# Performance work log

Hardware: AMD Instinct MI355X
Metric: run time of the kernel (lower is better)

The kernel has to match this reference:

```python
import jax, jax.numpy as jnp
import numpy as np

B, T, C = 8, 1024, 1024
H, D = 16, 64  # num_heads, head_size

def setup_inputs() -> dict:
    key = jax.random.key(0)
    ks = jax.random.split(key, 6)
    s = C ** -0.5
    return {
        "x": jax.random.normal(ks[0], (B, T, C), dtype=jnp.float32),
        "Wq": jax.random.normal(ks[1], (H, C, D), dtype=jnp.float32) * s,
        "Wk": jax.random.normal(ks[2], (H, C, D), dtype=jnp.float32) * s,
        "Wv": jax.random.normal(ks[3], (H, C, D), dtype=jnp.float32) * s,
        "Wproj": jax.random.normal(ks[4], (H * D, C), dtype=jnp.float32) * ((H * D) ** -0.5),
        "bproj": jnp.zeros((C,), dtype=jnp.float32),
    }

def reference(x, Wq, Wk, Wv, Wproj, bproj):
    # per-head QKV projections, batched over heads via einsum (same math as looped heads)
    q = jnp.einsum('btc,hcd->bhtd', x, Wq)
    k = jnp.einsum('btc,hcd->bhtd', x, Wk)
    v = jnp.einsum('btc,hcd->bhtd', x, Wv)
    scale = D ** -0.5  # k.shape[-1]**-0.5 in original head
    scores = jnp.einsum('bhtd,bhsd->bhts', q, k) * scale  # [B,H,T,T]
    Tn = x.shape[1]
    causal = jnp.tril(jnp.ones((Tn, Tn), dtype=bool))
    scores = jnp.where(causal, scores, jnp.float32(-jnp.inf))
    att = jax.nn.softmax(scores, axis=-1)
    out = jnp.einsum('bhts,bhsd->bhtd', att, v)          # [B,H,T,D]
    out = out.transpose(0, 2, 1, 3).reshape(x.shape[0], Tn, H * D)  # concat heads
    return out @ Wproj + bproj  # dropout is identity at p=0.0
```

## Files before the change

### kernel.cpp

```cpp
#include <hip/hip_runtime.h>
#include <hip/hip_bf16.h>

#define B_ 8
#define T_ 1024
#define C_ 1024
#define H_ 16
#define D_ 64
#define QKVLD 3072

typedef short v8s __attribute__((ext_vector_type(8)));
typedef float v4f __attribute__((ext_vector_type(4)));

__device__ __forceinline__ unsigned short f2b(float f) {
    unsigned int u = __builtin_bit_cast(unsigned int, f);
    unsigned int lsb = (u >> 16) & 1u;
    u += 0x7fffu + lsb;
    return (unsigned short)(u >> 16);
}

__device__ __forceinline__ float fexp2(float x) {
#if __has_builtin(__builtin_amdgcn_exp2f)
    return __builtin_amdgcn_exp2f(x);
#else
    return __expf(x * 0.69314718056f);
#endif
}

#define GLOAD16(gp, lp)                                                          \
    __builtin_amdgcn_global_load_lds(                                            \
        (const __attribute__((address_space(1))) unsigned int*)(gp),             \
        (__attribute__((address_space(3))) unsigned int*)(lp), 16, 0, 0)

#define VMWAIT() __asm__ volatile("s_waitcnt vmcnt(0)" ::: "memory")

__global__ void cast_x_kernel(const float* __restrict__ x, unsigned short* __restrict__ y, int n) {
    int i = (blockIdx.x * 256 + threadIdx.x) * 4;
    if (i < n) {
        float4 v = *(const float4*)(x + i);
        ushort4 o;
        o.x = f2b(v.x); o.y = f2b(v.y); o.z = f2b(v.z); o.w = f2b(v.w);
        *(ushort4*)(y + i) = o;
    }
}

__global__ void transpose_wqkv(const float* __restrict__ Wq, const float* __restrict__ Wk,
                               const float* __restrict__ Wv, unsigned short* __restrict__ WqkvT) {
    int z = blockIdx.y;
    int h = z / 3, part = z % 3;
    const float* src = (part == 0 ? Wq : (part == 1 ? Wk : Wv)) + (size_t)h * C_ * D_;
    int c0 = blockIdx.x * 64;
    __shared__ unsigned short t[64][65];
    for (int i = threadIdx.x; i < 4096; i += 256) {
        int r = i >> 6, d = i & 63;
        t[d][r] = f2b(src[(size_t)(c0 + r) * D_ + d]);
    }
    __syncthreads();
    unsigned short* dst = WqkvT + (size_t)(h * 192 + part * 64) * C_;
    for (int i = threadIdx.x; i < 4096; i += 256) {
        int d = i >> 6, r = i & 63;
        dst[(size_t)d * C_ + c0 + r] = t[d][r];
    }
}

__global__ void transpose_wproj(const float* __restrict__ W, unsigned short* __restrict__ Wt) {
    int k0 = blockIdx.y * 64, n0 = blockIdx.x * 64;
    __shared__ unsigned short t[64][65];
    for (int i = threadIdx.x; i < 4096; i += 256) {
        int r = i >> 6, c = i & 63;
        t[c][r] = f2b(W[(size_t)(k0 + r) * C_ + n0 + c]);
    }
    __syncthreads();
    for (int i = threadIdx.x; i < 4096; i += 256) {
        int n = i >> 6, k = i & 63;
        Wt[(size_t)(n0 + n) * 1024 + k0 + k] = t[n][k];
    }
}

template<int WRITE_MODE>
__global__ __launch_bounds__(256) void gemm_bt(const unsigned short* __restrict__ A,
                                               const unsigned short* __restrict__ Bt,
                                               void* __restrict__ Cout,
                                               const float* __restrict__ bias,
                                               int M, int N, int K) {
    __shared__ unsigned short lA[128 * 32];
    __shared__ unsigned short lB[128 * 32];
    int tid = threadIdx.x;
    int m0 = blockIdx.y * 128, n0 = blockIdx.x * 128;
    int lane = tid & 63, w = tid >> 6;
    int quad = lane >> 4, l16 = lane & 15;
    int wm = w >> 1, wn = w & 1;

    const unsigned short* gA[2];
    const unsigned short* gB[2];
    int ldsOff[2];
    #pragma unroll
    for (int j = 0; j < 2; j++) {
        int c = j * 256 + tid;
        int row = c >> 2;
        int col8 = ((c & 3) ^ ((row >> 1) & 3)) * 8;
        gA[j] = A + (size_t)(m0 + row) * K + col8;
        gB[j] = Bt + (size_t)(n0 + row) * K + col8;
        ldsOff[j] = (j * 256 + w * 64) * 16;
    }
    int rcol = (quad ^ ((l16 >> 1) & 3)) * 8;

    v4f acc[4][4];
    #pragma unroll
    for (int i = 0; i < 4; i++)
        #pragma unroll
        for (int j = 0; j < 4; j++) acc[i][j] = (v4f){0.f, 0.f, 0.f, 0.f};

    for (int k0 = 0; k0 < K; k0 += 32) {
        #pragma unroll
        for (int j = 0; j < 2; j++) {
            GLOAD16(gA[j] + k0, (char*)lA + ldsOff[j]);
            GLOAD16(gB[j] + k0, (char*)lB + ldsOff[j]);
        }
        VMWAIT();
        __syncthreads();
        v8s af[4], bf[4];
        #pragma unroll
        for (int mt = 0; mt < 4; mt++) af[mt] = *(const v8s*)&lA[(wm * 64 + mt * 16 + l16) * 32 + rcol];
        #pragma unroll
        for (int nt = 0; nt < 4; nt++) bf[nt] = *(const v8s*)&lB[(wn * 64 + nt * 16 + l16) * 32 + rcol];
        #pragma unroll
        for (int mt = 0; mt < 4; mt++)
            #pragma unroll
            for (int nt = 0; nt < 4; nt++)
                acc[mt][nt] = __builtin_amdgcn_mfma_f32_16x16x32_bf16(af[mt], bf[nt], acc[mt][nt], 0, 0, 0);
        __syncthreads();
    }
    #pragma unroll
    for (int mt = 0; mt < 4; mt++) {
        #pragma unroll
        for (int nt = 0; nt < 4; nt++) {
            #pragma unroll
            for (int r = 0; r < 4; r++) {
                int row = m0 + wm * 64 + mt * 16 + quad * 4 + r;
                int col = n0 + wn * 64 + nt * 16 + l16;
                float v = acc[mt][nt][r];
                if (WRITE_MODE == 1)
                    ((float*)Cout)[(size_t)row * N + col] = v + bias[col];
                else
                    ((unsigned short*)Cout)[(size_t)row * N + col] = f2b(v);
            }
        }
    }
}

__global__ void transpose_v(const unsigned short* __restrict__ QKV, unsigned short* __restrict__ Vt) {
    int t0 = blockIdx.x * 64;
    int bh = blockIdx.y;
    int b = bh >> 4, h = bh & 15;
    __shared__ unsigned short t[64][65];
    for (int i = threadIdx.x; i < 4096; i += 256) {
        int r = i >> 6, d = i & 63;
        t[d][r] = QKV[(size_t)(b * T_ + t0 + r) * QKVLD + h * 192 + 128 + d];
    }
    __syncthreads();
    for (int i = threadIdx.x; i < 4096; i += 256) {
        int d = i >> 6, r = i & 63;
        Vt[((size_t)bh * 64 + d) * T_ + t0 + r] = t[d][r];
    }
}

__global__ __launch_bounds__(256) void attn_kernel(const unsigned short* __restrict__ QKV,
                                                   const unsigned short* __restrict__ Vt,
                                                   unsigned short* __restrict__ Ob) {
    int bh = blockIdx.x;
    int qt = 7 - blockIdx.y;
    int b = bh >> 4, h = bh & 15;
    int tid = threadIdx.x, lane = tid & 63, w = tid >> 6;
    int quad = lane >> 4, l16 = lane & 15;
    int qg0 = qt * 128 + w * 32;

    __shared__ unsigned short lK[2][2][64][32];
    __shared__ unsigned short lV[2][64][32];
    __shared__ unsigned short lP[4][32][76];

    v8s aq[2][2];
    #pragma unroll
    for (int st = 0; st < 2; st++) {
        const unsigned short* qp = QKV + (size_t)(b * T_ + qg0 + st * 16 + l16) * QKVLD + h * 192;
        aq[st][0] = *(const v8s*)(qp + quad * 8);
        aq[st][1] = *(const v8s*)(qp + 32 + quad * 8);
    }

    const unsigned short* gK[2];
    const unsigned short* gV[2];
    int ldsOff[2];
    #pragma unroll
    for (int j = 0; j < 2; j++) {
        int c = j * 256 + tid;
        int halfp = c >> 8, row = (c >> 2) & 63;
        int col8 = ((c & 3) ^ ((row >> 1) & 3)) * 8;
        gK[j] = QKV + (size_t)(b * T_ + row) * QKVLD + h * 192 + 64 + halfp * 32 + col8;
        gV[j] = Vt + ((size_t)bh * 64 + row) * T_ + halfp * 32 + col8;
        ldsOff[j] = (j * 256 + w * 64) * 16;
    }
    int rcol = (quad ^ ((l16 >> 1) & 3)) * 8;

    v4f accO[2][4];
    float lsum[2][4];
    #pragma unroll
    for (int st = 0; st < 2; st++)
        #pragma unroll
        for (int i = 0; i < 4; i++) { accO[st][i] = (v4f){0.f, 0.f, 0.f, 0.f}; lsum[st][i] = 0.f; }

    int ntiles = 2 * qt + 2;
    const float SC = 0.1803368801f;

    #pragma unroll
    for (int j = 0; j < 2; j++)
        GLOAD16(gK[j], (char*)&lK[0][0][0][0] + ldsOff[j]);

    for (int it = 0; it < ntiles; it++) {
        int cur = it & 1, nxt = cur ^ 1;
        int s0 = it * 64;
        __asm__ volatile("s_waitcnt vmcnt(0)" ::: "memory");
        __asm__ volatile("s_barrier" ::: "memory");
        #pragma unroll
        for (int j = 0; j < 2; j++)
            GLOAD16(gV[j] + s0, (char*)&lV[0][0][0] + ldsOff[j]);
        __asm__ volatile("" ::: "memory");
        {
            int itn = (it + 1 < ntiles) ? it + 1 : it;
            size_t koff = (size_t)itn * 64 * QKVLD;
            #pragma unroll
            for (int j = 0; j < 2; j++)
                GLOAD16(gK[j] + koff, (char*)&lK[nxt][0][0][0] + ldsOff[j]);
        }
        bool act0 = (qg0 + 15 >= s0);
        bool act1 = (qg0 + 31 >= s0);
        if (act1) {
            v4f sf[2][4];
            #pragma unroll
            for (int nt = 0; nt < 4; nt++) {
                v8s bk0 = *(const v8s*)&lK[cur][0][nt * 16 + l16][rcol];
                v8s bk1 = *(const v8s*)&lK[cur][1][nt * 16 + l16][rcol];
                if (act0) {
                    v4f a = (v4f){0.f, 0.f, 0.f, 0.f};
                    a = __builtin_amdgcn_mfma_f32_16x16x32_bf16(aq[0][0], bk0, a, 0, 0, 0);
                    a = __builtin_amdgcn_mfma_f32_16x16x32_bf16(aq[0][1], bk1, a, 0, 0, 0);
                    sf[0][nt] = a;
                }
                v4f a1 = (v4f){0.f, 0.f, 0.f, 0.f};
                a1 = __builtin_amdgcn_mfma_f32_16x16x32_bf16(aq[1][0], bk0, a1, 0, 0, 0);
                a1 = __builtin_amdgcn_mfma_f32_16x16x32_bf16(aq[1][1], bk1, a1, 0, 0, 0);
                sf[1][nt] = a1;
            }
            bool diag = (it >= ntiles - 2);
            #pragma unroll
            for (int st = 0; st < 2; st++) {
                if (st == 0 && !act0) continue;
                if (diag) {
                    #pragma unroll
                    for (int nt = 0; nt < 4; nt++)
                        #pragma unroll
                        for (int r = 0; r < 4; r++) {
                            int sg = s0 + nt * 16 + l16;
                            int qg = qg0 + st * 16 + quad * 4 + r;
                            float p = (sg > qg) ? 0.f : fexp2(sf[st][nt][r] * SC);
                            lsum[st][r] += p;
                            lP[w][st * 16 + quad * 4 + r][nt * 16 + l16] = f2b(p);
                        }
                } else {
                    #pragma unroll
                    for (int nt = 0; nt < 4; nt++)
                        #pragma unroll
                        for (int r = 0; r < 4; r++) {
                            float p = fexp2(sf[st][nt][r] * SC);
                            lsum[st][r] += p;
                            lP[w][st * 16 + quad * 4 + r][nt * 16 + l16] = f2b(p);
                        }
                }
            }
        }
        __asm__ volatile("s_waitcnt vmcnt(2)" ::: "memory");
        __asm__ volatile("s_barrier" ::: "memory");
        __asm__ volatile("s_waitcnt lgkmcnt(0)" ::: "memory");
        if (act1) {
            #pragma unroll
            for (int sc = 0; sc < 2; sc++) {
                v8s ap0, ap1;
                if (act0) ap0 = *(const v8s*)&lP[w][l16][sc * 32 + quad * 8];
                ap1 = *(const v8s*)&lP[w][16 + l16][sc * 32 + quad * 8];
                #pragma unroll
                for (int dt = 0; dt < 4; dt++) {
                    v8s bv = *(const v8s*)&lV[sc][dt * 16 + l16][rcol];
                    if (act0) accO[0][dt] = __builtin_amdgcn_mfma_f32_16x16x32_bf16(ap0, bv, accO[0][dt], 0, 0, 0);
                    accO[1][dt] = __builtin_amdgcn_mfma_f32_16x16x32_bf16(ap1, bv, accO[1][dt], 0, 0, 0);
                }
            }
        }
    }
    #pragma unroll
    for (int st = 0; st < 2; st++)
        #pragma unroll
        for (int r = 0; r < 4; r++) {
            float s = lsum[st][r];
            #pragma unroll
            for (int off = 1; off < 16; off <<= 1) s += __shfl_xor(s, off, 64);
            float inv = 1.0f / s;
            int q = qg0 + st * 16 + quad * 4 + r;
            #pragma unroll
            for (int dt = 0; dt < 4; dt++) {
                int d = dt * 16 + l16;
                Ob[(size_t)(b * T_ + q) * (H_ * D_) + h * 64 + d] = f2b(accO[st][dt][r] * inv);
            }
        }
}

extern "C" void kernel_launch(void* const* d_in, const int* in_sizes, int n_in,
                              void* d_out, int out_size, void* d_ws, size_t ws_size,
                              hipStream_t stream) {
    const float* x     = (const float*)d_in[0];
    const float* Wq    = (const float*)d_in[1];
    const float* Wk    = (const float*)d_in[2];
    const float* Wv    = (const float*)d_in[3];
    const float* Wproj = (const float*)d_in[4];
    const float* bproj = (const float*)d_in[5];
    float* out = (float*)d_out;

    char* ws = (char*)d_ws;
    unsigned short* xb     = (unsigned short*)ws;
    unsigned short* WqkvT  = (unsigned short*)(ws + 16777216);
    unsigned short* WprojT = (unsigned short*)(ws + 23068672);
    unsigned short* QKV    = (unsigned short*)(ws + 25165824);
    unsigned short* Vt     = (unsigned short*)(ws + 75497472);
    unsigned short* Ob     = (unsigned short*)(ws + 92274688);

    cast_x_kernel<<<dim3(8192), dim3(256), 0, stream>>>(x, xb, B_ * T_ * C_);
    transpose_wqkv<<<dim3(16, 48), dim3(256), 0, stream>>>(Wq, Wk, Wv, WqkvT);
    transpose_wproj<<<dim3(16, 16), dim3(256), 0, stream>>>(Wproj, WprojT);
    gemm_bt<0><<<dim3(24, 64), dim3(256), 0, stream>>>(xb, WqkvT, QKV, nullptr, 8192, 3072, 1024);
    transpose_v<<<dim3(16, 128), dim3(256), 0, stream>>>(QKV, Vt);
    attn_kernel<<<dim3(128, 8), dim3(256), 0, stream>>>(QKV, Vt, Ob);
    gemm_bt<1><<<dim3(8, 64), dim3(256), 0, stream>>>(Ob, WprojT, out, bproj, 8192, 1024, 1024);
}
```

Measured before the change: 252.4 us.

## Rework GEMM with 256x128 tiles, 32x32 MFMA, and double-buffered LDS prefetch

The bf16 GEMM used for the QKV and output projections now uses 256x128 block tiles, with each wave computing 128x64 through 32x32x16 MFMA instructions instead of 16x16x32. Global-to-LDS loads are double-buffered, so the next K tile is fetched while the current one is computed, and one barrier per iteration replaces the previous load-wait-compute-sync sequence. The aim is more operand reuse per LDS read and less exposed global-load latency. In exchange it uses more accumulator registers, which launch_bounds(256,2) constrains, and launches half as many blocks.

After: 266.0 us. 1.05x slower.

```diff
diff --git a/kernel.cpp b/kernel.cpp
--- a/kernel.cpp
+++ b/kernel.cpp
@@ -10,6 +10,7 @@
 
 typedef short v8s __attribute__((ext_vector_type(8)));
 typedef float v4f __attribute__((ext_vector_type(4)));
+typedef float v16f __attribute__((ext_vector_type(16)));
 
 __device__ __forceinline__ unsigned short f2b(float f) {
     unsigned int u = __builtin_bit_cast(unsigned int, f);
@@ -30,8 +31,6 @@
     __builtin_amdgcn_global_load_lds(                                            \
         (const __attribute__((address_space(1))) unsigned int*)(gp),             \
         (__attribute__((address_space(3))) unsigned int*)(lp), 16, 0, 0)
-
-#define VMWAIT() __asm__ volatile("s_waitcnt vmcnt(0)" ::: "memory")
 
 __global__ void cast_x_kernel(const float* __restrict__ x, unsigned short* __restrict__ y, int n) {
     int i = (blockIdx.x * 256 + threadIdx.x) * 4;
@@ -77,68 +76,97 @@
 }
 
 template<int WRITE_MODE>
-__global__ __launch_bounds__(256) void gemm_bt(const unsigned short* __restrict__ A,
-                                               const unsigned short* __restrict__ Bt,
-                                               void* __restrict__ Cout,
-                                               const float* __restrict__ bias,
-                                               int M, int N, int K) {
-    __shared__ unsigned short lA[128 * 32];
-    __shared__ unsigned short lB[128 * 32];
+__global__ __launch_bounds__(256, 2) void gemm_bt(const unsigned short* __restrict__ A,
+                                                  const unsigned short* __restrict__ Bt,
+                                                  void* __restrict__ Cout,
+                                                  const float* __restrict__ bias,
+                                                  int M, int N, int K) {
+    __shared__ unsigned short lA[2][256 * 32];
+    __shared__ unsigned short lB[2][128 * 32];
     int tid = threadIdx.x;
-    int m0 = blockIdx.y * 128, n0 = blockIdx.x * 128;
+    int m0 = blockIdx.y * 256, n0 = blockIdx.x * 128;
     int lane = tid & 63, w = tid >> 6;
-    int quad = lane >> 4, l16 = lane & 15;
+    int half = lane >> 5, l32 = lane & 31;
     int wm = w >> 1, wn = w & 1;
 
-    const unsigned short* gA[2];
+    const unsigned short* gA[4];
+    int offA[4];
+    #pragma unroll
+    for (int j = 0; j < 4; j++) {
+        int c = j * 256 + tid;
+        int row = c >> 2;
+        int col8 = ((c & 3) ^ ((row >> 1) & 3)) * 8;
+        gA[j] = A + (size_t)(m0 + row) * K + col8;
+        offA[j] = (j * 256 + w * 64) * 16;
+    }
     const unsigned short* gB[2];
-    int ldsOff[2];
+    int offB[2];
     #pragma unroll
     for (int j = 0; j < 2; j++) {
         int c = j * 256 + tid;
         int row = c >> 2;
         int col8 = ((c & 3) ^ ((row >> 1) & 3)) * 8;
-        gA[j] = A + (size_t)(m0 + row) * K + col8;
         gB[j] = Bt + (size_t)(n0 + row) * K + col8;
-        ldsOff[j] = (j * 256 + w * 64) * 16;
-    }
-    int rcol = (quad ^ ((l16 >> 1) & 3)) * 8;
-
-    v4f acc[4][4];
-    #pragma unroll
-    for (int i = 0; i < 4; i++)
-        #pragma unroll
-        for (int j = 0; j < 4; j++) acc[i][j] = (v4f){0.f, 0.f, 0.f, 0.f};
-
-    for (int k0 = 0; k0 < K; k0 += 32) {
-        #pragma unroll
-        for (int j = 0; j < 2; j++) {
-            GLOAD16(gA[j] + k0, (char*)lA + ldsOff[j]);
-            GLOAD16(gB[j] + k0, (char*)lB + ldsOff[j]);
-        }
-        VMWAIT();
-        __syncthreads();
-        v8s af[4], bf[4];
-        #pragma unroll
-        for (int mt = 0; mt < 4; mt++) af[mt] = *(const v8s*)&lA[(wm * 64 + mt * 16 + l16) * 32 + rcol];
-        #pragma unroll
-        for (int nt = 0; nt < 4; nt++) bf[nt] = *(const v8s*)&lB[(wn * 64 + nt * 16 + l16) * 32 + rcol];
-        #pragma unroll
-        for (int mt = 0; mt < 4; mt++)
-            #pragma unroll
-            for (int nt = 0; nt < 4; nt++)
-                acc[mt][nt] = __builtin_amdgcn_mfma_f32_16x16x32_bf16(af[mt], bf[nt], acc[mt][nt], 0, 0, 0);
-        __syncthreads();
-    }
-    #pragma unroll
-    for (int mt = 0; mt < 4; mt++) {
-        #pragma unroll
-        for (int nt = 0; nt < 4; nt++) {
-            #pragma unroll
-            for (int r = 0; r < 4; r++) {
-                int row = m0 + wm * 64 + mt * 16 + quad * 4 + r;
-                int col = n0 + wn * 64 + nt * 16 + l16;
-                float v = acc[mt][nt][r];
+        offB[j] = (j * 256 + w * 64) * 16;
+    }
+
+    int am[4], bn[2];
+    #pragma unroll
+    for (int mi = 0; mi < 4; mi++) am[mi] = wm * 128 + mi * 32 + l32;
+    #pragma unroll
+    for (int ni = 0; ni < 2; ni++) bn[ni] = wn * 64 + ni * 32 + l32;
+
+    v16f acc[4][2];
+    #pragma unroll
+    for (int mi = 0; mi < 4; mi++)
+        #pragma unroll
+        for (int ni = 0; ni < 2; ni++)
+            #pragma unroll
+            for (int r = 0; r < 16; r++) acc[mi][ni][r] = 0.f;
+
+    int ktiles = K >> 5;
+    #pragma unroll
+    for (int j = 0; j < 4; j++) GLOAD16(gA[j], (char*)&lA[0][0] + offA[j]);
+    #pragma unroll
+    for (int j = 0; j < 2; j++) GLOAD16(gB[j], (char*)&lB[0][0] + offB[j]);
+
+    for (int it = 0; it < ktiles; it++) {
+        int cur = it & 1, nxt = cur ^ 1;
+        __asm__ volatile("s_waitcnt vmcnt(0)" ::: "memory");
+        __asm__ volatile("s_barrier" ::: "memory");
+        {
+            int kn = (it + 1 < ktiles) ? (it + 1) * 32 : it * 32;
+            #pragma unroll
+            for (int j = 0; j < 4; j++) GLOAD16(gA[j] + kn, (char*)&lA[nxt][0] + offA[j]);
+            #pragma unroll
+            for (int j = 0; j < 2; j++) GLOAD16(gB[j] + kn, (char*)&lB[nxt][0] + offB[j]);
+        }
+        #pragma unroll
+        for (int step = 0; step < 2; step++) {
+            int g = step * 2 + half;
+            v8s af[4], bf[2];
+            #pragma unroll
+            for (int mi = 0; mi < 4; mi++)
+                af[mi] = *(const v8s*)&lA[cur][am[mi] * 32 + ((g ^ ((am[mi] >> 1) & 3)) * 8)];
+            #pragma unroll
+            for (int ni = 0; ni < 2; ni++)
+                bf[ni] = *(const v8s*)&lB[cur][bn[ni] * 32 + ((g ^ ((bn[ni] >> 1) & 3)) * 8)];
+            #pragma unroll
+            for (int mi = 0; mi < 4; mi++)
+                #pragma unroll
+                for (int ni = 0; ni < 2; ni++)
+                    acc[mi][ni] = __builtin_amdgcn_mfma_f32_32x32x16_bf16(af[mi], bf[ni], acc[mi][ni], 0, 0, 0);
+        }
+    }
+    #pragma unroll
+    for (int mi = 0; mi < 4; mi++) {
+        #pragma unroll
+        for (int ni = 0; ni < 2; ni++) {
+            int col = n0 + wn * 64 + ni * 32 + l32;
+            #pragma unroll
+            for (int r = 0; r < 16; r++) {
+                int row = m0 + wm * 128 + mi * 32 + (r & 3) + 8 * (r >> 2) + 4 * half;
+                float v = acc[mi][ni][r];
                 if (WRITE_MODE == 1)
                     ((float*)Cout)[(size_t)row * N + col] = v + bias[col];
                 else
@@ -333,8 +361,8 @@
     cast_x_kernel<<<dim3(8192), dim3(256), 0, stream>>>(x, xb, B_ * T_ * C_);
     transpose_wqkv<<<dim3(16, 48), dim3(256), 0, stream>>>(Wq, Wk, Wv, WqkvT);
     transpose_wproj<<<dim3(16, 16), dim3(256), 0, stream>>>(Wproj, WprojT);
-    gemm_bt<0><<<dim3(24, 64), dim3(256), 0, stream>>>(xb, WqkvT, QKV, nullptr, 8192, 3072, 1024);
+    gemm_bt<0><<<dim3(24, 32), dim3(256), 0, stream>>>(xb, WqkvT, QKV, nullptr, 8192, 3072, 1024);
     transpose_v<<<dim3(16, 128), dim3(256), 0, stream>>>(QKV, Vt);
     attn_kernel<<<dim3(128, 8), dim3(256), 0, stream>>>(QKV, Vt, Ob);
-    gemm_bt<1><<<dim3(8, 64), dim3(256), 0, stream>>>(Ob, WprojT, out, bproj, 8192, 1024, 1024);
-}
+    gemm_bt<1><<<dim3(8, 32), dim3(256), 0, stream>>>(Ob, WprojT, out, bproj, 8192, 1024, 1024);
+}
```
